# Performance work log

Measured on AMD Instinct MI355X. Metric: run time of the kernel, lower is better.

The kernel has to match this reference:

```python
import jax, jax.numpy as jnp
import numpy as np

B, C, H, W = 16, 3, 512, 512
K = 15            # PSF support
BALANCE = 0.1     # skimage wiener 'balance' regularization weight


def _ir2tf(ir, h, w):
    """skimage uft.ir2tf: zero-pad impulse response at origin, circular-shift
    so its center sits at (0,0), then real FFT. Works with leading batch dims."""
    kh, kw = ir.shape[-2], ir.shape[-1]
    padded = jnp.zeros(ir.shape[:-2] + (h, w), ir.dtype)
    padded = padded.at[..., :kh, :kw].set(ir)
    padded = jnp.roll(padded, shift=(-(kh // 2), -(kw // 2)), axis=(-2, -1))
    return jnp.fft.rfft2(padded)


def _laplacian_tf(h, w, dtype):
    # skimage uft.laplacian impulse response for ndim=2
    impr = jnp.array([[0.0, -1.0, 0.0],
                      [-1.0, 4.0, -1.0],
                      [0.0, -1.0, 0.0]], dtype=dtype)
    return _ir2tf(impr, h, w)


def setup_inputs() -> dict:
    key = jax.random.key(0)
    k1, k2 = jax.random.split(key)
    y = jax.random.normal(k1, (B, C, H, W), dtype=jnp.float32)
    filters = jax.random.uniform(k2, (B, C, K, K), dtype=jnp.float32)
    # normalize PSFs to sum to 1 (realistic blur kernels)
    filters = filters / jnp.sum(filters, axis=(-2, -1), keepdims=True)
    return {"y": y, "filters": filters}


def reference(y, filters):
    h, w = y.shape[-2], y.shape[-1]
    trans_func = _ir2tf(filters, h, w)                 # [B,C,H,W//2+1] complex
    reg = _laplacian_tf(h, w, y.dtype)                 # [H,W//2+1] complex
    denom = jnp.abs(trans_func) ** 2 + BALANCE * jnp.abs(reg) ** 2
    wiener_filter = jnp.conj(trans_func) / denom
    x = jnp.fft.irfft2(wiener_filter * jnp.fft.rfft2(y), s=(h, w))
    # skimage wiener clip=True default
    return jnp.clip(x, -1.0, 1.0).astype(y.dtype)
```

## Files before the change

### kernel.cpp

```cpp
#include <hip/hip_runtime.h>
#include <cstddef>
#include <cmath>

#define FFT_N    512
#define IMG_PIX  (FFT_N * FFT_N)
#define NIMG     48
#define NPAIR    24
#define KSZ      15
#define KK       (KSZ * KSZ)
#define BAL      0.1f
#define TWO_PI   6.283185307179586f
#define NV       257
#define PLANE    ((size_t)FFT_N * NV)
#define EXSZ     576

__device__ __forceinline__ float2 cadd(float2 a, float2 b) { return make_float2(a.x + b.x, a.y + b.y); }
__device__ __forceinline__ float2 csub(float2 a, float2 b) { return make_float2(a.x - b.x, a.y - b.y); }
__device__ __forceinline__ float2 cmul(float2 a, float2 b) {
  return make_float2(a.x * b.x - a.y * b.y, a.x * b.y + a.y * b.x);
}
__device__ __forceinline__ int ex1(int c, int b, int g) { return 72 * c + 8 * b + g; }
__device__ __forceinline__ int ex2(int c, int e, int g) { return 72 * c + 9 * e + g; }

__device__ __forceinline__ void wsync() {
  asm volatile("" ::: "memory");
  __builtin_amdgcn_wave_barrier();
  asm volatile("" ::: "memory");
}

template <bool INV>
__device__ __forceinline__ void dft8(float2 r[8]) {
  const float RH = 0.70710678118654752440f;
  float2 s0 = cadd(r[0], r[4]), s1 = cadd(r[1], r[5]), s2 = cadd(r[2], r[6]), s3 = cadd(r[3], r[7]);
  float2 d0 = csub(r[0], r[4]), d1 = csub(r[1], r[5]), d2 = csub(r[2], r[6]), d3 = csub(r[3], r[7]);
  if (!INV) {
    d1 = make_float2(RH * (d1.x + d1.y), RH * (d1.y - d1.x));
    d2 = make_float2(d2.y, -d2.x);
    d3 = make_float2(RH * (d3.y - d3.x), RH * (-d3.x - d3.y));
  } else {
    d1 = make_float2(RH * (d1.x - d1.y), RH * (d1.x + d1.y));
    d2 = make_float2(-d2.y, d2.x);
    d3 = make_float2(RH * (-d3.x - d3.y), RH * (d3.x - d3.y));
  }
  float2 t0 = cadd(s0, s2), t1 = csub(s0, s2), t2 = cadd(s1, s3), t3 = csub(s1, s3);
  t3 = INV ? make_float2(-t3.y, t3.x) : make_float2(t3.y, -t3.x);
  float2 E0 = cadd(t0, t2), E1 = cadd(t1, t3), E2 = csub(t0, t2), E3 = csub(t1, t3);
  t0 = cadd(d0, d2); t1 = csub(d0, d2); t2 = cadd(d1, d3); t3 = csub(d1, d3);
  t3 = INV ? make_float2(-t3.y, t3.x) : make_float2(t3.y, -t3.x);
  r[0] = E0; r[2] = E1; r[4] = E2; r[6] = E3;
  r[1] = cadd(t0, t2); r[3] = cadd(t1, t3); r[5] = csub(t0, t2); r[7] = csub(t1, t3);
}

template <bool INV>
__device__ void fft512_reg(float2 r[8], float* ere, float* eim, const float2* tw, int j) {
  const int hi = j >> 3, lo = j & 7;
  dft8<INV>(r);
  #pragma unroll
  for (int c = 1; c < 8; ++c) {
    float2 w = tw[(8 * hi * c) & 511];
    if (INV) w.y = -w.y;
    r[c] = cmul(r[c], w);
  }
  #pragma unroll
  for (int c = 0; c < 8; ++c) { int a = ex1(c, hi, lo); ere[a] = r[c].x; eim[a] = r[c].y; }
  wsync();
  #pragma unroll
  for (int b = 0; b < 8; ++b) { int a = ex1(hi, b, lo); r[b] = make_float2(ere[a], eim[a]); }
  dft8<INV>(r);
  {
    float2 base = tw[(lo * hi) & 511];
    float2 step = tw[(8 * lo) & 511];
    if (INV) { base.y = -base.y; step.y = -step.y; }
    #pragma unroll
    for (int e = 0; e < 8; ++e) { r[e] = cmul(r[e], base); base = cmul(base, step); }
  }
  wsync();
  #pragma unroll
  for (int e = 0; e < 8; ++e) { int a = ex2(hi, e, lo); ere[a] = r[e].x; eim[a] = r[e].y; }
  wsync();
  #pragma unroll
  for (int g = 0; g < 8; ++g) { int a = ex2(hi, lo, g); r[g] = make_float2(ere[a], eim[a]); }
  dft8<INV>(r);
}

__device__ __forceinline__ void bitswap_lanes(float2 r[8], int j) {
  int src = ((j & 7) << 3) | (j >> 3);
  #pragma unroll
  for (int f = 0; f < 8; ++f) {
    r[f].x = __shfl(r[f].x, src);
    r[f].y = __shfl(r[f].y, src);
  }
}

__device__ __forceinline__ void fill_tw(float2* tw, int t) {
  float s, c;
  float ang = -TWO_PI * (float)t / (float)FFT_N;
  sincosf(ang, &s, &c); tw[t] = make_float2(c, s);
  ang = -TWO_PI * (float)(t + 256) / (float)FFT_N;
  sincosf(ang, &s, &c); tw[t + 256] = make_float2(c, s);
}

__global__ __launch_bounds__(256) void k_psf(
    const float* __restrict__ filters, float2* __restrict__ St) {
  __shared__ float fs[KK];
  int img = blockIdx.x;
  int t = threadIdx.x;
  if (t < KK) fs[t] = filters[(size_t)img * KK + t];
  __syncthreads();
  for (int v = t; v < NV; v += 256) {
    float cs[KSZ], sn[KSZ];
    #pragma unroll
    for (int jj = 0; jj < KSZ; ++jj) {
      float ang = -TWO_PI * (float)(v * (jj - 7)) / (float)FFT_N;
      sincosf(ang, &sn[jj], &cs[jj]);
    }
    float2* dst = St + ((size_t)img * NV + v) * KSZ;
    #pragma unroll
    for (int i = 0; i < KSZ; ++i) {
      float2 s = make_float2(0.f, 0.f);
      #pragma unroll
      for (int jj = 0; jj < KSZ; ++jj) {
        float fv = fs[i * KSZ + jj];
        s.x += fv * cs[jj];
        s.y += fv * sn[jj];
      }
      dst[i] = s;
    }
  }
}

__global__ __launch_bounds__(256) void k_rows_fwd(
    const float* __restrict__ y, float2* __restrict__ zh1, int pairBase) {
  __shared__ float ere[4][EXSZ], eim[4][EXSZ];
  __shared__ float2 tw[512];
  int t = threadIdx.x;
  int w = __builtin_amdgcn_readfirstlane(t >> 6);
  int j = t & 63;
  fill_tw(tw, t);
  __syncthreads();
  int p = blockIdx.x >> 5, bg = blockIdx.x & 31;
  int gp = pairBase + p;
  const float* baseA = y + (size_t)(2 * gp) * IMG_PIX;
  const float* baseB = baseA + IMG_PIX;
  float2* plA = zh1 + (size_t)(2 * p) * PLANE;
  float2* plB = plA + PLANE;
  for (int q = 0; q < 4; ++q) {
    int row = bg * 16 + q * 4 + w;
    const float* rA = baseA + (size_t)row * FFT_N;
    const float* rB = baseB + (size_t)row * FFT_N;
    float2 r[8];
    #pragma unroll
    for (int a = 0; a < 8; ++a) r[a] = make_float2(rA[64 * a + j], rB[64 * a + j]);
    fft512_reg<false>(r, ere[w], eim[w], tw, j);
    bitswap_lanes(r, j);
    float2 m[8];
    int msrc = (64 - j) & 63;
    #pragma unroll
    for (int f = 0; f < 8; ++f) { m[f].x = __shfl(r[f].x, msrc); m[f].y = __shfl(r[f].y, msrc); }
    float2* wA = plA + (size_t)row * NV;
    float2* wB = plB + (size_t)row * NV;
    #pragma unroll
    for (int f = 0; f < 5; ++f) {
      int v = 64 * f + j;
      float2 Zp = r[f];
      float2 Zm = (j == 0) ? m[(8 - f) & 7] : m[7 - f];
      float2 ya = make_float2(0.5f * (Zp.x + Zm.x), 0.5f * (Zp.y - Zm.y));
      float2 yb = make_float2(0.5f * (Zp.y + Zm.y), 0.5f * (Zm.x - Zp.x));
      if (v <= 256) { wA[v] = ya; wB[v] = yb; }
    }
  }
}

__global__ __launch_bounds__(256) void k_transpose(
    const float2* __restrict__ src, float2* __restrict__ dst, int H, int W) {
  __shared__ float2 tile[32][33];
  size_t po = (size_t)blockIdx.z * H * W;
  const float2* s = src + po;
  float2* d = dst + po;
  int tx = threadIdx.x & 31, ty = threadIdx.x >> 5;
  int w0 = blockIdx.x * 32, h0 = blockIdx.y * 32;
  #pragma unroll
  for (int k = 0; k < 4; ++k) {
    int h = h0 + ty + 8 * k, ww = w0 + tx;
    if (h < H && ww < W) tile[ty + 8 * k][tx] = s[(size_t)h * W + ww];
  }
  __syncthreads();
  #pragma unroll
  for (int k = 0; k < 4; ++k) {
    int wr = w0 + ty + 8 * k, hr = h0 + tx;
    if (wr < W && hr < H) d[(size_t)wr * H + hr] = tile[tx][ty + 8 * k];
  }
}

__global__ __launch_bounds__(256) void k_col_wiener(
    float2* __restrict__ zh2, const float2* __restrict__ St, int imgBase) {
  __shared__ float ere[4][EXSZ], eim[4][EXSZ];
  __shared__ float2 tw[512];
  int t = threadIdx.x;
  int w = __builtin_amdgcn_readfirstlane(t >> 6);
  int j = t & 63;
  fill_tw(tw, t);
  __syncthreads();
  int img_l = blockIdx.x / 17, vg = blockIdx.x % 17;
  int img = imgBase + img_l;
  const float SC = 1.f / (float)IMG_PIX;
  for (int q = 0; q < 4; ++q) {
    int v = vg * 16 + w * 4 + q;
    bool ok = (v <= 256);
    float2* col = zh2 + ((size_t)img_l * NV + (ok ? v : 0)) * FFT_N;
    float2 r[8];
    #pragma unroll
    for (int a = 0; a < 8; ++a) r[a] = ok ? col[64 * a + j] : make_float2(0.f, 0.f);
    fft512_reg<false>(r, ere[w], eim[w], tw, j);
    if (ok) {
      const float2* sp = St + ((size_t)img * NV + v) * KSZ;
      int u0 = (j >> 3) + 8 * (j & 7);
      float2 G[8];
      #pragma unroll
      for (int m = 0; m < 8; ++m) G[m] = make_float2(0.f, 0.f);
      #pragma unroll
      for (int i = 0; i < KSZ; ++i) {
        float2 wb = tw[(u0 * (i - 7)) & 511];
        float2 b = cmul(sp[i], wb);
        int m = (i + 1) & 7;
        G[m] = cadd(G[m], b);
      }
      dft8<false>(G);
      float lv = 2.f - 2.f * tw[v].x;
      #pragma unroll
      for (int f = 0; f < 8; ++f) {
        int u = u0 + 64 * f;
        float2 H = G[f];
        float lap = (2.f - 2.f * tw[u].x) + lv;
        float inv = SC / (H.x * H.x + H.y * H.y + BAL * lap * lap);
        float2 Z = r[f];
        r[f] = make_float2((H.x * Z.x + H.y * Z.y) * inv,
                           (H.x * Z.y - H.y * Z.x) * inv);
      }
    }
    bitswap_lanes(r, j);
    fft512_reg<true>(r, ere[w], eim[w], tw, j);
    bitswap_lanes(r, j);
    if (ok) {
      #pragma unroll
      for (int f = 0; f < 8; ++f) col[64 * f + j] = r[f];
    }
  }
}

__global__ __launch_bounds__(256) void k_rows_inv(
    const float2* __restrict__ zh1, float* __restrict__ out, int pairBase) {
  __shared__ float ere[4][EXSZ], eim[4][EXSZ];
  __shared__ float2 tw[512];
  int t = threadIdx.x;
  int w = __builtin_amdgcn_readfirstlane(t >> 6);
  int j = t & 63;
  fill_tw(tw, t);
  __syncthreads();
  int p = blockIdx.x >> 5, bg = blockIdx.x & 31;
  int gp = pairBase + p;
  const float2* plA = zh1 + (size_t)(2 * p) * PLANE;
  const float2* plB = plA + PLANE;
  float* baseA = out + (size_t)(2 * gp) * IMG_PIX;
  float* baseB = baseA + IMG_PIX;
  for (int q = 0; q < 4; ++q) {
    int row = bg * 16 + q * 4 + w;
    const float2* rA = plA + (size_t)row * NV;
    const float2* rB = plB + (size_t)row * NV;
    float2 r[8];
    #pragma unroll
    for (int a = 0; a < 8; ++a) {
      int n = 64 * a + j;
      if (n <= 256) {
        float2 ya = rA[n], yb = rB[n];
        r[a] = make_float2(ya.x - yb.y, ya.y + yb.x);
      } else {
        int n2 = 512 - n;
        float2 ya = rA[n2], yb = rB[n2];
        r[a] = make_float2(ya.x + yb.y, yb.x - ya.y);
      }
    }
    fft512_reg<true>(r, ere[w], eim[w], tw, j);
    bitswap_lanes(r, j);
    float* oA = baseA + (size_t)row * FFT_N;
    float* oB = baseB + (size_t)row * FFT_N;
    #pragma unroll
    for (int f = 0; f < 8; ++f) {
      int px = 64 * f + j;
      oA[px] = fminf(1.f, fmaxf(-1.f, r[f].x));
      oB[px] = fminf(1.f, fmaxf(-1.f, r[f].y));
    }
  }
}

extern "C" void kernel_launch(void* const* d_in, const int* in_sizes, int n_in,
                              void* d_out, int out_size, void* d_ws, size_t ws_size,
                              hipStream_t stream) {
  const float* y       = (const float*)d_in[0];
  const float* filters = (const float*)d_in[1];
  float* out = (float*)d_out;

  size_t sElems = (size_t)NIMG * NV * KSZ;
  float2* St = (float2*)d_ws;
  size_t sBytes = sElems * sizeof(float2);
  size_t zBytes = (ws_size > sBytes) ? (ws_size - sBytes) : 0;
  size_t perPair = 4 * PLANE * sizeof(float2);
  int chunk = (int)(zBytes / perPair);
  if (chunk > NPAIR) chunk = NPAIR;
  if (chunk < 1)     chunk = 1;
  float2* zh1 = St + sElems;
  float2* zh2 = zh1 + (size_t)chunk * 2 * PLANE;

  k_psf<<<NIMG, 256, 0, stream>>>(filters, St);

  for (int p0 = 0; p0 < NPAIR; p0 += chunk) {
    int nc = (chunk < NPAIR - p0) ? chunk : (NPAIR - p0);
    k_rows_fwd  <<<nc * 32, 256, 0, stream>>>(y, zh1, p0);
    k_transpose <<<dim3(9, 16, 2 * nc), 256, 0, stream>>>(zh1, zh2, FFT_N, NV);
    k_col_wiener<<<2 * nc * 17, 256, 0, stream>>>(zh2, St, 2 * p0);
    k_transpose <<<dim3(16, 9, 2 * nc), 256, 0, stream>>>(zh2, zh1, NV, FFT_N);
    k_rows_inv  <<<nc * 32, 256, 0, stream>>>(zh1, out, p0);
  }
}
```

Before: 195.3 us.

## Fuse transposes into column Wiener kernel via shared-memory tiled column loads

Removes the two standalone transpose kernels. The column FFT kernel now reads 16 columns of the row-major spectrum directly through a shared-memory tile and writes them back the same way. The intermediate row stride is padded to 264 so rows stay aligned, and only one scratch buffer is needed, which halves per-pair workspace and may allow larger chunks. In exchange each column block does strided 128-byte-segment global accesses and holds 32 complex values per thread in registers, which raises register pressure.

```diff
diff --git a/kernel.cpp b/kernel.cpp
--- a/kernel.cpp
+++ b/kernel.cpp
@@ -11,7 +11,8 @@
 #define BAL      0.1f
 #define TWO_PI   6.283185307179586f
 #define NV       257
-#define PLANE    ((size_t)FFT_N * NV)
+#define RS       264
+#define PLANE    ((size_t)FFT_N * RS)
 #define EXSZ     576
 
 __device__ __forceinline__ float2 cadd(float2 a, float2 b) { return make_float2(a.x + b.x, a.y + b.y); }
@@ -130,7 +131,7 @@
 }
 
 __global__ __launch_bounds__(256) void k_rows_fwd(
-    const float* __restrict__ y, float2* __restrict__ zh1, int pairBase) {
+    const float* __restrict__ y, float2* __restrict__ zh, int pairBase) {
   __shared__ float ere[4][EXSZ], eim[4][EXSZ];
   __shared__ float2 tw[512];
   int t = threadIdx.x;
@@ -142,7 +143,7 @@
   int gp = pairBase + p;
   const float* baseA = y + (size_t)(2 * gp) * IMG_PIX;
   const float* baseB = baseA + IMG_PIX;
-  float2* plA = zh1 + (size_t)(2 * p) * PLANE;
+  float2* plA = zh + (size_t)(2 * p) * PLANE;
   float2* plB = plA + PLANE;
   for (int q = 0; q < 4; ++q) {
     int row = bg * 16 + q * 4 + w;
@@ -157,8 +158,8 @@
     int msrc = (64 - j) & 63;
     #pragma unroll
     for (int f = 0; f < 8; ++f) { m[f].x = __shfl(r[f].x, msrc); m[f].y = __shfl(r[f].y, msrc); }
-    float2* wA = plA + (size_t)row * NV;
-    float2* wB = plB + (size_t)row * NV;
+    float2* wA = plA + (size_t)row * RS;
+    float2* wB = plB + (size_t)row * RS;
     #pragma unroll
     for (int f = 0; f < 5; ++f) {
       int v = 64 * f + j;
@@ -171,48 +172,50 @@
   }
 }
 
-__global__ __launch_bounds__(256) void k_transpose(
-    const float2* __restrict__ src, float2* __restrict__ dst, int H, int W) {
-  __shared__ float2 tile[32][33];
-  size_t po = (size_t)blockIdx.z * H * W;
-  const float2* s = src + po;
-  float2* d = dst + po;
-  int tx = threadIdx.x & 31, ty = threadIdx.x >> 5;
-  int w0 = blockIdx.x * 32, h0 = blockIdx.y * 32;
-  #pragma unroll
-  for (int k = 0; k < 4; ++k) {
-    int h = h0 + ty + 8 * k, ww = w0 + tx;
-    if (h < H && ww < W) tile[ty + 8 * k][tx] = s[(size_t)h * W + ww];
-  }
-  __syncthreads();
-  #pragma unroll
-  for (int k = 0; k < 4; ++k) {
-    int wr = w0 + ty + 8 * k, hr = h0 + tx;
-    if (wr < W && hr < H) d[(size_t)wr * H + hr] = tile[tx][ty + 8 * k];
-  }
-}
-
 __global__ __launch_bounds__(256) void k_col_wiener(
-    float2* __restrict__ zh2, const float2* __restrict__ St, int imgBase) {
+    float2* __restrict__ zh, const float2* __restrict__ St, int imgBase) {
   __shared__ float ere[4][EXSZ], eim[4][EXSZ];
   __shared__ float2 tw[512];
+  __shared__ float tre[64][17], tim[64][17];
   int t = threadIdx.x;
   int w = __builtin_amdgcn_readfirstlane(t >> 6);
   int j = t & 63;
   fill_tw(tw, t);
-  __syncthreads();
   int img_l = blockIdx.x / 17, vg = blockIdx.x % 17;
   int img = imgBase + img_l;
+  int vbase = vg * 16;
+  int ncols = (vg == 16) ? 1 : 16;
+  float2* pl = zh + (size_t)img_l * PLANE;
   const float SC = 1.f / (float)IMG_PIX;
+  int vi = t & 15, ri0 = t >> 4;
+  float2 rq[4][8];
+  __syncthreads();
+  #pragma unroll
+  for (int a = 0; a < 8; ++a) {
+    #pragma unroll
+    for (int rr = 0; rr < 4; ++rr) {
+      int ri = ri0 + 16 * rr;
+      if (vi < ncols) {
+        float2 z = pl[(size_t)(64 * a + ri) * RS + vbase + vi];
+        tre[ri][vi] = z.x; tim[ri][vi] = z.y;
+      }
+    }
+    __syncthreads();
+    #pragma unroll
+    for (int q = 0; q < 4; ++q) {
+      int c = w * 4 + q;
+      int cc = (c < ncols) ? c : 0;
+      rq[q][a] = make_float2(tre[j][cc], tim[j][cc]);
+    }
+    __syncthreads();
+  }
+  #pragma unroll
   for (int q = 0; q < 4; ++q) {
-    int v = vg * 16 + w * 4 + q;
-    bool ok = (v <= 256);
-    float2* col = zh2 + ((size_t)img_l * NV + (ok ? v : 0)) * FFT_N;
-    float2 r[8];
-    #pragma unroll
-    for (int a = 0; a < 8; ++a) r[a] = ok ? col[64 * a + j] : make_float2(0.f, 0.f);
-    fft512_reg<false>(r, ere[w], eim[w], tw, j);
+    int c = w * 4 + q;
+    int v = vbase + c;
+    bool ok = (v <= 256) && (c < ncols);
     if (ok) {
+      fft512_reg<false>(rq[q], ere[w], eim[w], tw, j);
       const float2* sp = St + ((size_t)img * NV + v) * KSZ;
       int u0 = (j >> 3) + 8 * (j & 7);
       float2 G[8];
@@ -233,23 +236,36 @@
         float2 H = G[f];
         float lap = (2.f - 2.f * tw[u].x) + lv;
         float inv = SC / (H.x * H.x + H.y * H.y + BAL * lap * lap);
-        float2 Z = r[f];
-        r[f] = make_float2((H.x * Z.x + H.y * Z.y) * inv,
-                           (H.x * Z.y - H.y * Z.x) * inv);
-      }
-    }
-    bitswap_lanes(r, j);
-    fft512_reg<true>(r, ere[w], eim[w], tw, j);
-    bitswap_lanes(r, j);
-    if (ok) {
-      #pragma unroll
-      for (int f = 0; f < 8; ++f) col[64 * f + j] = r[f];
-    }
+        float2 Z = rq[q][f];
+        rq[q][f] = make_float2((H.x * Z.x + H.y * Z.y) * inv,
+                               (H.x * Z.y - H.y * Z.x) * inv);
+      }
+      bitswap_lanes(rq[q], j);
+      fft512_reg<true>(rq[q], ere[w], eim[w], tw, j);
+      bitswap_lanes(rq[q], j);
+    }
+  }
+  #pragma unroll
+  for (int f = 0; f < 8; ++f) {
+    #pragma unroll
+    for (int q = 0; q < 4; ++q) {
+      int c = w * 4 + q;
+      if (c < ncols && vbase + c <= 256) { tre[j][c] = rq[q][f].x; tim[j][c] = rq[q][f].y; }
+    }
+    __syncthreads();
+    #pragma unroll
+    for (int rr = 0; rr < 4; ++rr) {
+      int ri = ri0 + 16 * rr;
+      if (vi < ncols) {
+        pl[(size_t)(64 * f + ri) * RS + vbase + vi] = make_float2(tre[ri][vi], tim[ri][vi]);
+      }
+    }
+    __syncthreads();
   }
 }
 
 __global__ __launch_bounds__(256) void k_rows_inv(
-    const float2* __restrict__ zh1, float* __restrict__ out, int pairBase) {
+    const float2* __restrict__ zh, float* __restrict__ out, int pairBase) {
   __shared__ float ere[4][EXSZ], eim[4][EXSZ];
   __shared__ float2 tw[512];
   int t = threadIdx.x;
@@ -259,14 +275,14 @@
   __syncthreads();
   int p = blockIdx.x >> 5, bg = blockIdx.x & 31;
   int gp = pairBase + p;
-  const float2* plA = zh1 + (size_t)(2 * p) * PLANE;
+  const float2* plA = zh + (size_t)(2 * p) * PLANE;
   const float2* plB = plA + PLANE;
   float* baseA = out + (size_t)(2 * gp) * IMG_PIX;
   float* baseB = baseA + IMG_PIX;
   for (int q = 0; q < 4; ++q) {
     int row = bg * 16 + q * 4 + w;
-    const float2* rA = plA + (size_t)row * NV;
-    const float2* rB = plB + (size_t)row * NV;
+    const float2* rA = plA + (size_t)row * RS;
+    const float2* rB = plB + (size_t)row * RS;
     float2 r[8];
     #pragma unroll
     for (int a = 0; a < 8; ++a) {
@@ -304,21 +320,18 @@
   float2* St = (float2*)d_ws;
   size_t sBytes = sElems * sizeof(float2);
   size_t zBytes = (ws_size > sBytes) ? (ws_size - sBytes) : 0;
-  size_t perPair = 4 * PLANE * sizeof(float2);
+  size_t perPair = 2 * PLANE * sizeof(float2);
   int chunk = (int)(zBytes / perPair);
   if (chunk > NPAIR) chunk = NPAIR;
   if (chunk < 1)     chunk = 1;
-  float2* zh1 = St + sElems;
-  float2* zh2 = zh1 + (size_t)chunk * 2 * PLANE;
+  float2* zh = St + sElems;
 
   k_psf<<<NIMG, 256, 0, stream>>>(filters, St);
 
   for (int p0 = 0; p0 < NPAIR; p0 += chunk) {
     int nc = (chunk < NPAIR - p0) ? chunk : (NPAIR - p0);
-    k_rows_fwd  <<<nc * 32, 256, 0, stream>>>(y, zh1, p0);
-    k_transpose <<<dim3(9, 16, 2 * nc), 256, 0, stream>>>(zh1, zh2, FFT_N, NV);
-    k_col_wiener<<<2 * nc * 17, 256, 0, stream>>>(zh2, St, 2 * p0);
-    k_transpose <<<dim3(16, 9, 2 * nc), 256, 0, stream>>>(zh2, zh1, NV, FFT_N);
-    k_rows_inv  <<<nc * 32, 256, 0, stream>>>(zh1, out, p0);
-  }
-}
+    k_rows_fwd  <<<nc * 32,     256, 0, stream>>>(y, zh, p0);
+    k_col_wiener<<<2 * nc * 17, 256, 0, stream>>>(zh, St, 2 * p0);
+    k_rows_inv  <<<nc * 32,     256, 0, stream>>>(zh, out, p0);
+  }
+}
```

Measured after the change: 173.1 us. 1.13x faster.
